# Kernel tuning notes

Hardware: AMD Instinct MI355X
Metric: run time of the kernel (lower is better)

The kernel has to match this reference:

```python
import jax, jax.numpy as jnp
import numpy as np

NEG_SLOPE = 0.2  # PyG GATConv leaky_relu slope


def _gat_layer(x, src, dst, W, a_src, a_dst, b, concat, num_nodes):
    # x: [N, F_in], W: [F_in, H*C], a_src/a_dst: [H, C], b: [H*C] or [C]
    H, C = a_src.shape
    h = (x @ W).reshape(num_nodes, H, C)                      # [N, H, C]
    s_src = jnp.einsum('nhc,hc->nh', h, a_src)                # [N, H]
    s_dst = jnp.einsum('nhc,hc->nh', h, a_dst)                # [N, H]
    e = jax.nn.leaky_relu(s_src[src] + s_dst[dst], NEG_SLOPE) # [E, H]
    # segment softmax over edges sharing a destination node
    m = jax.ops.segment_max(e, dst, num_segments=num_nodes)
    m = jnp.where(jnp.isfinite(m), m, 0.0)
    p = jnp.exp(e - m[dst])
    z = jax.ops.segment_sum(p, dst, num_segments=num_nodes)
    alpha = p / (z[dst] + 1e-16)                              # [E, H]
    msg = h[src] * alpha[:, :, None]                          # [E, H, C]
    out = jax.ops.segment_sum(msg, dst, num_segments=num_nodes)  # [N, H, C]
    out = out.reshape(num_nodes, H * C) if concat else out.mean(axis=1)
    return out + b


def setup_inputs() -> dict:
    key = jax.random.key(0)
    ks = jax.random.split(key, 16)
    N, E, F = 100000, 800000, 128
    H, C = 4, 32
    sc_in = 1.0 / np.sqrt(F)
    inp = {
        'x': jax.random.normal(ks[0], (N, F), jnp.float32),
        'edge_index': jax.random.randint(ks[1], (2, E), 0, N, jnp.int64),
        'W1': jax.random.normal(ks[2], (F, H * C), jnp.float32) * sc_in,
        'a_src1': jax.random.normal(ks[3], (H, C), jnp.float32),
        'a_dst1': jax.random.normal(ks[4], (H, C), jnp.float32),
        'b1': jax.random.normal(ks[5], (H * C,), jnp.float32) * 0.01,
        'W2': jax.random.normal(ks[6], (F, H * C), jnp.float32) * sc_in,
        'a_src2': jax.random.normal(ks[7], (H, C), jnp.float32),
        'a_dst2': jax.random.normal(ks[8], (H, C), jnp.float32),
        'b2': jax.random.normal(ks[9], (H * C,), jnp.float32) * 0.01,
        'W3': jax.random.normal(ks[10], (F, H * F), jnp.float32) * sc_in,
        'a_src3': jax.random.normal(ks[11], (H, F), jnp.float32),
        'a_dst3': jax.random.normal(ks[12], (H, F), jnp.float32),
        'b3': jax.random.normal(ks[13], (F,), jnp.float32) * 0.01,
    }
    return inp


def reference(x, edge_index, W1, a_src1, a_dst1, b1, W2, a_src2, a_dst2, b2,
              W3, a_src3, a_dst3, b3):
    N = x.shape[0]
    # PyG GATConv default: add self loops
    loop = jnp.arange(N, dtype=edge_index.dtype)
    src = jnp.concatenate([edge_index[0], loop])
    dst = jnp.concatenate([edge_index[1], loop])
    # conv1 (concat heads) + residual + ELU
    x1 = jax.nn.elu(_gat_layer(x, src, dst, W1, a_src1, a_dst1, b1, True, N) + x)
    # intermediate conv (concat heads) + residual + ELU
    x2 = jax.nn.elu(_gat_layer(x1, src, dst, W2, a_src2, a_dst2, b2, True, N) + x1)
    # final conv (mean over heads) + residual, no ELU
    x3 = _gat_layer(x2, src, dst, W3, a_src3, a_dst3, b3, False, N) + x2
    return x3
```

## Files before the change

kernel.cpp:

```cpp
#include <hip/hip_runtime.h>
#include <hip/hip_bf16.h>
#include <cstdint>

#define NEG_SLOPE 0.2f

typedef __bf16 bf16x8 __attribute__((ext_vector_type(8)));
typedef _Float16 half8 __attribute__((ext_vector_type(8)));
typedef float  floatx4 __attribute__((ext_vector_type(4)));

__device__ __forceinline__ float us2f(unsigned short u) {
    union { unsigned int i; float f; } c; c.i = ((unsigned int)u) << 16; return c.f;
}
__device__ __forceinline__ unsigned short f2us(float f) {
    union { float f; unsigned int i; } c; c.f = f;
    unsigned int x = c.i;
    unsigned int r = (x + 0x7fffu + ((x >> 16) & 1u)) >> 16;
    return (unsigned short)r;
}
__device__ __forceinline__ unsigned short f2h(float f) {
    union { _Float16 h; unsigned short u; } c; c.h = (_Float16)f; return c.u;
}
__device__ __forceinline__ float h2f(unsigned short u) {
    union { _Float16 h; unsigned short u; } c; c.u = u; return (float)c.h;
}
__device__ __forceinline__ float ldx(const void* p, int i, int bf) {
    return bf ? us2f(((const unsigned short*)p)[i]) : ((const float*)p)[i];
}
__device__ __forceinline__ void split2(float f, unsigned short& h, unsigned short& l) {
    h = f2us(f);
    l = f2us(f - us2f(h));
}
__device__ __forceinline__ float sel4(const float* a, int i) {
    float lo = (i & 1) ? a[1] : a[0];
    float hi = (i & 1) ? a[3] : a[2];
    return (i & 2) ? hi : lo;
}
__device__ __forceinline__ void fma4(float w, uint2 u,
                                     float& a0, float& a1, float& a2, float& a3) {
    union { unsigned int i; float f; } t0, t1, t2, t3;
    t0.i = u.x << 16; t1.i = u.x & 0xffff0000u;
    t2.i = u.y << 16; t3.i = u.y & 0xffff0000u;
    a0 = fmaf(w, t0.f, a0); a1 = fmaf(w, t1.f, a1);
    a2 = fmaf(w, t2.f, a2); a3 = fmaf(w, t3.f, a3);
}

__global__ void k_detect(const unsigned short* __restrict__ x16,
                         const unsigned int* __restrict__ ei,
                         int* __restrict__ flags) {
    if (threadIdx.x == 0 && blockIdx.x == 0) {
        int cnt = 0;
        for (int i = 0; i < 1024; ++i) {
            const unsigned short u = x16[2 * i];
            const int e = (u >> 7) & 0xFF;
            if (e < 100 || e > 160) ++cnt;
        }
        flags[0] = (cnt < 256) ? 1 : 0;
        int is64 = 1;
        for (int i = 0; i < 64; ++i)
            if (ei[2 * i + 1] != 0u) { is64 = 0; break; }
        flags[1] = is64;
    }
}

__device__ __forceinline__ int edge_at(const void* ei, int f64, long long idx) {
    if (f64) return (int)((const long long*)ei)[idx];
    return ((const int*)ei)[idx];
}

__global__ void k_hist(const void* __restrict__ ei, const int* __restrict__ flags,
                       int* __restrict__ deg, int E, int N) {
    const int f64 = flags[1];
    const int EP = E + N;
    for (int e = blockIdx.x * blockDim.x + threadIdx.x; e < EP; e += gridDim.x * blockDim.x) {
        int dst = (e < E) ? edge_at(ei, f64, (long long)E + e) : (e - E);
        atomicAdd(&deg[dst], 1);
    }
}

__global__ __launch_bounds__(1024) void k_scan_a(const int* __restrict__ deg,
                                                 int* __restrict__ coff,
                                                 int* __restrict__ part, int N) {
    __shared__ int tmp[1024];
    const int t = threadIdx.x, idx = blockIdx.x * 1024 + t;
    const int v = (idx < N) ? deg[idx] : 0;
    tmp[t] = v; __syncthreads();
    for (int s = 1; s < 1024; s <<= 1) {
        int a = (t >= s) ? tmp[t - s] : 0;
        __syncthreads(); tmp[t] += a; __syncthreads();
    }
    if (idx < N) coff[idx] = tmp[t] - v;
    if (t == 1023) part[blockIdx.x] = tmp[1023];
}

__global__ __launch_bounds__(1024) void k_scan_b(int* __restrict__ part,
                                                 int* __restrict__ coff, int nblk, int N) {
    __shared__ int tmp[1024];
    const int t = threadIdx.x;
    const int v = (t < nblk) ? part[t] : 0;
    tmp[t] = v; __syncthreads();
    for (int s = 1; s < 1024; s <<= 1) {
        int a = (t >= s) ? tmp[t - s] : 0;
        __syncthreads(); tmp[t] += a; __syncthreads();
    }
    if (t < nblk) part[t] = tmp[t] - v;
    if (t == 1023) coff[N] = tmp[1023];
}

__global__ __launch_bounds__(1024) void k_scan_c(int* __restrict__ coff,
                                                 const int* __restrict__ part, int N) {
    const int idx = blockIdx.x * 1024 + threadIdx.x;
    if (idx < N) coff[idx] += part[blockIdx.x];
}

__global__ void k_scatter(const void* __restrict__ ei, const int* __restrict__ flags,
                          const int* __restrict__ coff, int* __restrict__ cpos,
                          int* __restrict__ csrc, int E, int N) {
    const int f64 = flags[1];
    const int EP = E + N;
    for (int e = blockIdx.x * blockDim.x + threadIdx.x; e < EP; e += gridDim.x * blockDim.x) {
        int src, dst;
        if (e < E) { src = edge_at(ei, f64, e); dst = edge_at(ei, f64, (long long)E + e); }
        else       { src = dst = e - E; }
        const int p = atomicAdd(&cpos[dst], 1);
        csrc[coff[dst] + p] = src;
    }
}

template <int F16>
__global__ void k_wfrag(const void* __restrict__ Wv, const int* __restrict__ flags,
                        int wstride, int total,
                        unsigned short* __restrict__ outH, unsigned short* __restrict__ outL) {
    const int bf = flags[0];
    for (int tid = blockIdx.x * blockDim.x + threadIdx.x; tid < total;
         tid += gridDim.x * blockDim.x) {
        const int j    = tid & 7;
        const int lane = (tid >> 3) & 63;
        const int ks   = (tid >> 9) & 3;
        const int ntg  = (tid >> 11) & 7;
        const int blk  = tid >> 14;
        const int k = ks * 32 + (lane >> 4) * 8 + j;
        const int c = blk * 128 + ntg * 16 + (lane & 15);
        const float v = ldx(Wv, k * wstride + c, bf);
        unsigned short h, l;
        if (F16) {
            h = f2h(v);
            l = f2h(v - h2f(h));
        } else {
            split2(v, h, l);
        }
        outH[tid] = h; outL[tid] = l;
    }
}

__global__ void k_wa(const void* __restrict__ W, const void* __restrict__ as,
                     const void* __restrict__ ad, const int* __restrict__ flags,
                     float* __restrict__ va) {
    const int bf = flags[0];
    const int t = blockIdx.x * blockDim.x + threadIdx.x;
    if (t >= 512) return;
    const int k = t >> 2, h = t & 3;
    float ss = 0.f, dd = 0.f;
    for (int c = 0; c < 128; ++c) {
        const float w = ldx(W, k * 512 + h * 128 + c, bf);
        ss = fmaf(w, ldx(as, h * 128 + c, bf), ss);
        dd = fmaf(w, ldx(ad, h * 128 + c, bf), dd);
    }
    va[k * 8 + h] = ss;
    va[k * 8 + 4 + h] = dd;
}

template <bool XRAW, int SC>
__global__ __launch_bounds__(256) void k_gemm(const void* __restrict__ Xv,
                                              const unsigned short* __restrict__ whfB,
                                              const unsigned short* __restrict__ wlfB,
                                              unsigned short* __restrict__ Y16, int ystride,
                                              float* __restrict__ ssrc,
                                              float* __restrict__ sdst,
                                              const void* __restrict__ a_src,
                                              const void* __restrict__ a_dst,
                                              const int* __restrict__ flags,
                                              int N) {
    __shared__ __align__(16) unsigned short Ah[64][136], Al[64][136];
    __shared__ float sred[2][4][SC ? 64 : 1];
    const int bf   = flags[0];
    const int t    = threadIdx.x;
    const int row0 = blockIdx.x * 64;
    const int hy   = blockIdx.y;
    const unsigned short* whf = whfB + hy * 16384;
    const unsigned short* wlf = wlfB + hy * 16384;
    const int ycol0 = hy * 128;
    const int wv   = t >> 6;
    const int lane = t & 63;
    const int quad = lane >> 4;
    const int l16  = lane & 15;

#pragma unroll
    for (int it = 0; it < 8; ++it) {
        const int id = it * 256 + t;
        const int r  = id >> 5;
        const int c  = (id & 31) * 4;
        const int gr = row0 + r;
        ushort4 h4 = make_ushort4(0, 0, 0, 0), l4 = make_ushort4(0, 0, 0, 0);
        if (gr < N) {
            if (XRAW && bf) {
                h4 = *(const ushort4*)&((const unsigned short*)Xv)[(size_t)gr * 128 + c];
            } else {
                const float4 f = *(const float4*)&((const float*)Xv)[(size_t)gr * 128 + c];
                split2(f.x, h4.x, l4.x); split2(f.y, h4.y, l4.y);
                split2(f.z, h4.z, l4.z); split2(f.w, h4.w, l4.w);
            }
        }
        *(ushort4*)&Ah[r][c] = h4;
        *(ushort4*)&Al[r][c] = l4;
    }
    __syncthreads();

    floatx4 acc[4][2];
#pragma unroll
    for (int mt = 0; mt < 4; ++mt)
#pragma unroll
        for (int nt = 0; nt < 2; ++nt) acc[mt][nt] = (floatx4){0.f, 0.f, 0.f, 0.f};

#pragma unroll
    for (int ks = 0; ks < 4; ++ks) {
        const int ko = ks * 32 + quad * 8;
        bf16x8 ah[4], al[4], bh[2], bl[2];
#pragma unroll
        for (int mt = 0; mt < 4; ++mt) ah[mt] = *(const bf16x8*)&Ah[mt * 16 + l16][ko];
        if (!(XRAW && bf)) {
#pragma unroll
            for (int mt = 0; mt < 4; ++mt) al[mt] = *(const bf16x8*)&Al[mt * 16 + l16][ko];
        }
#pragma unroll
        for (int nt = 0; nt < 2; ++nt)
            bh[nt] = *(const bf16x8*)&whf[(((wv * 2 + nt) * 4 + ks) * 64 + lane) * 8];
        if (!bf) {
#pragma unroll
            for (int nt = 0; nt < 2; ++nt)
                bl[nt] = *(const bf16x8*)&wlf[(((wv * 2 + nt) * 4 + ks) * 64 + lane) * 8];
        }
#pragma unroll
        for (int mt = 0; mt < 4; ++mt)
#pragma unroll
            for (int nt = 0; nt < 2; ++nt) {
                acc[mt][nt] = __builtin_amdgcn_mfma_f32_16x16x32_bf16(ah[mt], bh[nt], acc[mt][nt], 0, 0, 0);
                if (!bf)
                    acc[mt][nt] = __builtin_amdgcn_mfma_f32_16x16x32_bf16(ah[mt], bl[nt], acc[mt][nt], 0, 0, 0);
                if (!(XRAW && bf))
                    acc[mt][nt] = __builtin_amdgcn_mfma_f32_16x16x32_bf16(al[mt], bh[nt], acc[mt][nt], 0, 0, 0);
            }
    }

    const int aBase = hy * 128 + wv * 32;
    float as_[2], ad_[2];
#pragma unroll
    for (int nt = 0; nt < 2; ++nt) {
        as_[nt] = ldx(a_src, aBase + nt * 16 + l16, bf);
        ad_[nt] = ldx(a_dst, aBase + nt * 16 + l16, bf);
    }

#pragma unroll
    for (int mt = 0; mt < 4; ++mt) {
        const int rl = mt * 16 + quad * 4;
#pragma unroll
        for (int r = 0; r < 4; ++r) {
            const int grow = row0 + rl + r;
            if (grow < N) {
#pragma unroll
                for (int nt = 0; nt < 2; ++nt)
                    Y16[(size_t)grow * ystride + ycol0 + wv * 32 + nt * 16 + l16] =
                        f2us(acc[mt][nt][r]);
            }
            float ps = acc[mt][0][r] * as_[0] + acc[mt][1][r] * as_[1];
            float pd = acc[mt][0][r] * ad_[0] + acc[mt][1][r] * ad_[1];
#pragma unroll
            for (int mk = 1; mk <= 8; mk <<= 1) {
                ps += __shfl_xor(ps, mk);
                pd += __shfl_xor(pd, mk);
            }
            if (SC == 0) {
                if (l16 == 0 && grow < N) {
                    ssrc[(size_t)grow * 4 + wv] = ps;
                    sdst[(size_t)grow * 4 + wv] = pd;
                }
            } else {
                if (l16 == 0) { sred[0][wv][rl + r] = ps; sred[1][wv][rl + r] = pd; }
            }
        }
    }
    if (SC == 1) {
        __syncthreads();
        if (t < 64 && row0 + t < N) {
            ssrc[(size_t)(row0 + t) * 4 + hy] = sred[0][0][t] + sred[0][1][t] + sred[0][2][t] + sred[0][3][t];
            sdst[(size_t)(row0 + t) * 4 + hy] = sred[1][0][t] + sred[1][1][t] + sred[1][2][t] + sred[1][3][t];
        }
    }
}

template <int MODE>
__global__ __launch_bounds__(256) void k_agg(const int* __restrict__ coff,
                                             const int* __restrict__ csrc,
                                             const float* __restrict__ ssrc,
                                             const float* __restrict__ sdst,
                                             const unsigned short* __restrict__ H16,
                                             const void* __restrict__ bias,
                                             const void* __restrict__ resid,
                                             const int* __restrict__ flags,
                                             void* __restrict__ out, int N,
                                             const float* __restrict__ va,
                                             float* __restrict__ ss2,
                                             float* __restrict__ sd2,
                                             unsigned short* __restrict__ x2h) {
    __shared__ int   sS[4][64];
    __shared__ float wS[4][256];
    __shared__ float vaS[(MODE == 1) ? 128 : 1][9];
    const int bf   = flags[0];
    const int wv   = threadIdx.x >> 6;
    const int lane = threadIdx.x & 63;
    const int n0   = blockIdx.x * 4 + wv;
    const bool nact = n0 < N;
    const int n    = nact ? n0 : (N - 1);
    const int beg = coff[n], end = coff[n + 1];
    const int deg = end - beg;

    if (MODE == 1) {
        for (int i = threadIdx.x; i < 1024; i += 256) vaS[i >> 3][i & 7] = va[i];
    }

    const float4 sdv = *(const float4*)&sdst[(size_t)n * 4];
    float sd[4] = { sdv.x, sdv.y, sdv.z, sdv.w };

    const bool fast = (deg <= 64);
    float m[4], z[4];

    if (fast) {
        const bool act = lane < deg;
        int myS = 0;
        float v[4];
#pragma unroll
        for (int h = 0; h < 4; ++h) v[h] = -1e30f;
        if (act) {
            myS = csrc[beg + lane];
            const float4 sp = *(const float4*)&ssrc[(size_t)myS * 4];
            const float s4[4] = { sp.x, sp.y, sp.z, sp.w };
#pragma unroll
            for (int h = 0; h < 4; ++h) {
                float tv = s4[h] + sd[h];
                v[h] = tv >= 0.f ? tv : NEG_SLOPE * tv;
            }
        }
#pragma unroll
        for (int h = 0; h < 4; ++h) m[h] = v[h];
#pragma unroll
        for (int mk = 1; mk <= 32; mk <<= 1)
#pragma unroll
            for (int h = 0; h < 4; ++h) m[h] = fmaxf(m[h], __shfl_xor(m[h], mk));
        float w[4];
#pragma unroll
        for (int h = 0; h < 4; ++h) w[h] = act ? expf(v[h] - m[h]) : 0.f;
#pragma unroll
        for (int h = 0; h < 4; ++h) z[h] = w[h];
#pragma unroll
        for (int mk = 1; mk <= 32; mk <<= 1)
#pragma unroll
            for (int h = 0; h < 4; ++h) z[h] += __shfl_xor(z[h], mk);
        if (act) {
            sS[wv][lane] = myS;
#pragma unroll
            for (int h = 0; h < 4; ++h)
                wS[wv][lane * 4 + h] = w[h] / (z[h] + 1e-16f);
        }
    } else {
#pragma unroll
        for (int h = 0; h < 4; ++h) m[h] = -1e30f;
        for (int e = beg + lane; e < end; e += 64) {
            const int s = csrc[e];
            const float4 sp = *(const float4*)&ssrc[(size_t)s * 4];
            const float s4[4] = { sp.x, sp.y, sp.z, sp.w };
#pragma unroll
            for (int h = 0; h < 4; ++h) {
                float tv = s4[h] + sd[h];
                tv = tv >= 0.f ? tv : NEG_SLOPE * tv;
                m[h] = fmaxf(m[h], tv);
            }
        }
#pragma unroll
        for (int mk = 1; mk <= 32; mk <<= 1)
#pragma unroll
            for (int h = 0; h < 4; ++h) m[h] = fmaxf(m[h], __shfl_xor(m[h], mk));
#pragma unroll
        for (int h = 0; h < 4; ++h) z[h] = 0.f;
        for (int e = beg + lane; e < end; e += 64) {
            const int s = csrc[e];
            const float4 sp = *(const float4*)&ssrc[(size_t)s * 4];
            const float s4[4] = { sp.x, sp.y, sp.z, sp.w };
#pragma unroll
            for (int h = 0; h < 4; ++h) {
                float tv = s4[h] + sd[h];
                tv = tv >= 0.f ? tv : NEG_SLOPE * tv;
                z[h] += expf(tv - m[h]);
            }
        }
#pragma unroll
        for (int mk = 1; mk <= 32; mk <<= 1)
#pragma unroll
            for (int h = 0; h < 4; ++h) z[h] += __shfl_xor(z[h], mk);
    }

    __syncthreads();

    const int half = lane >> 5;
    const int l32  = lane & 31;
    const int c4   = l32 * 4;
    const int hd   = l32 >> 3;
    float a0 = 0.f, a1 = 0.f, a2 = 0.f, a3 = 0.f;

    if (fast) {
        for (int e0 = 0; e0 < deg; e0 += 2) {
            const int e = e0 + half;
            if (e < deg) {
                const int s = sS[wv][e];
                const float w = wS[wv][e * 4 + hd];
                const uint2 u = *(const uint2*)&H16[(size_t)s * 128 + c4];
                fma4(w, u, a0, a1, a2, a3);
            }
        }
    } else {
        float ivh[4];
#pragma unroll
        for (int h = 0; h < 4; ++h) ivh[h] = 1.f / (z[h] + 1e-16f);
        const float mh = sel4(m, hd), sdh = sel4(sd, hd), ih = sel4(ivh, hd);
        for (int e0 = 0; e0 < deg; e0 += 2) {
            const int e = e0 + half;
            if (e < deg) {
                const int s = csrc[beg + e];
                float tv = ssrc[(size_t)s * 4 + hd] + sdh;
                tv = tv >= 0.f ? tv : NEG_SLOPE * tv;
                const float w = expf(tv - mh) * ih;
                const uint2 u = *(const uint2*)&H16[(size_t)s * 128 + c4];
                fma4(w, u, a0, a1, a2, a3);
            }
        }
    }

    a0 += __shfl_xor(a0, 32);
    a1 += __shfl_xor(a1, 32);
    a2 += __shfl_xor(a2, 32);
    a3 += __shfl_xor(a3, 32);

    if (half != 0 || !nact) return;
    const int ob = n * 128 + c4;
    const float vv[4] = { a0, a1, a2, a3 };
    float rr[4];
    if (MODE == 0) {
#pragma unroll
        for (int i = 0; i < 4; ++i) rr[i] = ldx(resid, ob + i, bf);
    } else {
        const float4 r4 = *(const float4*)&((const float*)resid)[ob];
        rr[0] = r4.x; rr[1] = r4.y; rr[2] = r4.z; rr[3] = r4.w;
    }
    float o[4];
#pragma unroll
    for (int i = 0; i < 4; ++i) {
        const float v = vv[i] + ldx(bias, c4 + i, bf) + rr[i];
        o[i] = v > 0.f ? v : expm1f(v);
    }
    float4 o4 = make_float4(o[0], o[1], o[2], o[3]);
    *(float4*)&((float*)out)[ob] = o4;

    if (MODE == 1) {
        ushort4 u16;
        u16.x = f2us(o[0]); u16.y = f2us(o[1]); u16.z = f2us(o[2]); u16.w = f2us(o[3]);
        *(ushort4*)&x2h[ob] = u16;
        float p[8];
#pragma unroll
        for (int o8 = 0; o8 < 8; ++o8)
            p[o8] = fmaf(o[0], vaS[c4 + 0][o8],
                    fmaf(o[1], vaS[c4 + 1][o8],
                    fmaf(o[2], vaS[c4 + 2][o8], o[3] * vaS[c4 + 3][o8])));
#pragma unroll
        for (int mk = 1; mk <= 16; mk <<= 1)
#pragma unroll
            for (int o8 = 0; o8 < 8; ++o8) p[o8] += __shfl_xor(p[o8], mk);
        if (l32 == 0) {
#pragma unroll
            for (int h = 0; h < 4; ++h) {
                ss2[(size_t)n * 4 + h] = p[h];
                sd2[(size_t)n * 4 + h] = p[4 + h];
            }
        }
    }
}

__global__ __launch_bounds__(256) void k_aggx(const int* __restrict__ coff,
                                              const int* __restrict__ csrc,
                                              const float* __restrict__ ssrc,
                                              const float* __restrict__ sdst,
                                              const unsigned short* __restrict__ X16,
                                              unsigned short* __restrict__ aggO,
                                              int N) {
    __shared__ int   sS[4][64];
    __shared__ float wS[4][256];
    const int wv   = threadIdx.x >> 6;
    const int lane = threadIdx.x & 63;
    const int n0   = blockIdx.x * 4 + wv;
    const bool nact = n0 < N;
    const int n    = nact ? n0 : (N - 1);
    const int beg = coff[n], end = coff[n + 1];
    const int deg = end - beg;

    const float4 sdv = *(const float4*)&sdst[(size_t)n * 4];
    float sd[4] = { sdv.x, sdv.y, sdv.z, sdv.w };

    const bool fast = (deg <= 64);
    float m[4], z[4];

    if (fast) {
        const bool act = lane < deg;
        int myS = 0;
        float v[4];
#pragma unroll
        for (int h = 0; h < 4; ++h) v[h] = -1e30f;
        if (act) {
            myS = csrc[beg + lane];
            const float4 sp = *(const float4*)&ssrc[(size_t)myS * 4];
            const float s4[4] = { sp.x, sp.y, sp.z, sp.w };
#pragma unroll
            for (int h = 0; h < 4; ++h) {
                float tv = s4[h] + sd[h];
                v[h] = tv >= 0.f ? tv : NEG_SLOPE * tv;
            }
        }
#pragma unroll
        for (int h = 0; h < 4; ++h) m[h] = v[h];
#pragma unroll
        for (int mk = 1; mk <= 32; mk <<= 1)
#pragma unroll
            for (int h = 0; h < 4; ++h) m[h] = fmaxf(m[h], __shfl_xor(m[h], mk));
        float w[4];
#pragma unroll
        for (int h = 0; h < 4; ++h) w[h] = act ? expf(v[h] - m[h]) : 0.f;
#pragma unroll
        for (int h = 0; h < 4; ++h) z[h] = w[h];
#pragma unroll
        for (int mk = 1; mk <= 32; mk <<= 1)
#pragma unroll
            for (int h = 0; h < 4; ++h) z[h] += __shfl_xor(z[h], mk);
        if (act) {
            sS[wv][lane] = myS;
#pragma unroll
            for (int h = 0; h < 4; ++h)
                wS[wv][lane * 4 + h] = w[h] / (z[h] + 1e-16f);
        }
    } else {
#pragma unroll
        for (int h = 0; h < 4; ++h) m[h] = -1e30f;
        for (int e = beg + lane; e < end; e += 64) {
            const int s = csrc[e];
            const float4 sp = *(const float4*)&ssrc[(size_t)s * 4];
            const float s4[4] = { sp.x, sp.y, sp.z, sp.w };
#pragma unroll
            for (int h = 0; h < 4; ++h) {
                float tv = s4[h] + sd[h];
                tv = tv >= 0.f ? tv : NEG_SLOPE * tv;
                m[h] = fmaxf(m[h], tv);
            }
        }
#pragma unroll
        for (int mk = 1; mk <= 32; mk <<= 1)
#pragma unroll
            for (int h = 0; h < 4; ++h) m[h] = fmaxf(m[h], __shfl_xor(m[h], mk));
#pragma unroll
        for (int h = 0; h < 4; ++h) z[h] = 0.f;
        for (int e = beg + lane; e < end; e += 64) {
            const int s = csrc[e];
            const float4 sp = *(const float4*)&ssrc[(size_t)s * 4];
            const float s4[4] = { sp.x, sp.y, sp.z, sp.w };
#pragma unroll
            for (int h = 0; h < 4; ++h) {
                float tv = s4[h] + sd[h];
                tv = tv >= 0.f ? tv : NEG_SLOPE * tv;
                z[h] += expf(tv - m[h]);
            }
        }
#pragma unroll
        for (int mk = 1; mk <= 32; mk <<= 1)
#pragma unroll
            for (int h = 0; h < 4; ++h) z[h] += __shfl_xor(z[h], mk);
    }

    __syncthreads();

    const int half = lane >> 5;
    const int l32  = lane & 31;
    const int c4   = l32 * 4;
    float ac[4][4];
#pragma unroll
    for (int h = 0; h < 4; ++h)
#pragma unroll
        for (int j = 0; j < 4; ++j) ac[h][j] = 0.f;

    if (fast) {
        for (int e0 = 0; e0 < deg; e0 += 2) {
            const int e = e0 + half;
            if (e < deg) {
                const int s = sS[wv][e];
                const float4 w4 = *(const float4*)&wS[wv][e * 4];
                const float wr[4] = { w4.x, w4.y, w4.z, w4.w };
                const uint2 u = *(const uint2*)&X16[(size_t)s * 128 + c4];
                union { unsigned int i; float f; } t0, t1, t2, t3;
                t0.i = u.x << 16; t1.i = u.x & 0xffff0000u;
                t2.i = u.y << 16; t3.i = u.y & 0xffff0000u;
#pragma unroll
                for (int h = 0; h < 4; ++h) {
                    ac[h][0] = fmaf(wr[h], t0.f, ac[h][0]);
                    ac[h][1] = fmaf(wr[h], t1.f, ac[h][1]);
                    ac[h][2] = fmaf(wr[h], t2.f, ac[h][2]);
                    ac[h][3] = fmaf(wr[h], t3.f, ac[h][3]);
                }
            }
        }
    } else {
        float ivh[4];
#pragma unroll
        for (int h = 0; h < 4; ++h) ivh[h] = 1.f / (z[h] + 1e-16f);
        for (int e0 = 0; e0 < deg; e0 += 2) {
            const int e = e0 + half;
            if (e < deg) {
                const int s = csrc[beg + e];
                const float4 sp = *(const float4*)&ssrc[(size_t)s * 4];
                const float s4[4] = { sp.x, sp.y, sp.z, sp.w };
                float wr[4];
#pragma unroll
                for (int h = 0; h < 4; ++h) {
                    float tv = s4[h] + sd[h];
                    tv = tv >= 0.f ? tv : NEG_SLOPE * tv;
                    wr[h] = expf(tv - m[h]) * ivh[h];
                }
                const uint2 u = *(const uint2*)&X16[(size_t)s * 128 + c4];
                union { unsigned int i; float f; } t0, t1, t2, t3;
                t0.i = u.x << 16; t1.i = u.x & 0xffff0000u;
                t2.i = u.y << 16; t3.i = u.y & 0xffff0000u;
#pragma unroll
                for (int h = 0; h < 4; ++h) {
                    ac[h][0] = fmaf(wr[h], t0.f, ac[h][0]);
                    ac[h][1] = fmaf(wr[h], t1.f, ac[h][1]);
                    ac[h][2] = fmaf(wr[h], t2.f, ac[h][2]);
                    ac[h][3] = fmaf(wr[h], t3.f, ac[h][3]);
                }
            }
        }
    }

#pragma unroll
    for (int h = 0; h < 4; ++h)
#pragma unroll
        for (int j = 0; j < 4; ++j) ac[h][j] += __shfl_xor(ac[h][j], 32);

    if (half != 0 || !nact) return;
#pragma unroll
    for (int h = 0; h < 4; ++h) {
        ushort4 o;
        o.x = f2h(ac[h][0]); o.y = f2h(ac[h][1]);
        o.z = f2h(ac[h][2]); o.w = f2h(ac[h][3]);
        *(ushort4*)&aggO[(size_t)n0 * 512 + h * 128 + c4] = o;
    }
}

__global__ __launch_bounds__(256) void k_gemm3(const unsigned short* __restrict__ A16,
                                               const unsigned short* __restrict__ whf,
                                               const unsigned short* __restrict__ wlf,
                                               const void* __restrict__ bias,
                                               const float* __restrict__ resid,
                                               const int* __restrict__ flags,
                                               void* __restrict__ out, int N) {
    __shared__ __align__(16) unsigned short Ah[64][136];
    const int bf   = flags[0];
    const int t    = threadIdx.x;
    const int row0 = blockIdx.x * 64;
    const int wv   = t >> 6;
    const int lane = t & 63;
    const int quad = lane >> 4;
    const int l16  = lane & 15;

    floatx4 acc[4][2];
#pragma unroll
    for (int mt = 0; mt < 4; ++mt)
#pragma unroll
        for (int nt = 0; nt < 2; ++nt) acc[mt][nt] = (floatx4){0.f, 0.f, 0.f, 0.f};

    for (int kc = 0; kc < 4; ++kc) {
        if (kc) __syncthreads();
#pragma unroll
        for (int it = 0; it < 8; ++it) {
            const int id = it * 256 + t;
            const int r  = id >> 5;
            const int c  = (id & 31) * 4;
            ushort4 h4 = make_ushort4(0, 0, 0, 0);
            if (row0 + r < N)
                h4 = *(const ushort4*)&A16[(size_t)(row0 + r) * 512 + kc * 128 + c];
            *(ushort4*)&Ah[r][c] = h4;
        }
        __syncthreads();

        const unsigned short* whc = whf + kc * 16384;
        const unsigned short* wlc = wlf + kc * 16384;
#pragma unroll
        for (int ks = 0; ks < 4; ++ks) {
            const int ko = ks * 32 + quad * 8;
            half8 ah[4], bh[2], bl[2];
#pragma unroll
            for (int mt = 0; mt < 4; ++mt) ah[mt] = *(const half8*)&Ah[mt * 16 + l16][ko];
#pragma unroll
            for (int nt = 0; nt < 2; ++nt) {
                bh[nt] = *(const half8*)&whc[(((wv * 2 + nt) * 4 + ks) * 64 + lane) * 8];
                bl[nt] = *(const half8*)&wlc[(((wv * 2 + nt) * 4 + ks) * 64 + lane) * 8];
            }
#pragma unroll
            for (int mt = 0; mt < 4; ++mt)
#pragma unroll
                for (int nt = 0; nt < 2; ++nt) {
                    acc[mt][nt] = __builtin_amdgcn_mfma_f32_16x16x32_f16(ah[mt], bh[nt], acc[mt][nt], 0, 0, 0);
                    acc[mt][nt] = __builtin_amdgcn_mfma_f32_16x16x32_f16(ah[mt], bl[nt], acc[mt][nt], 0, 0, 0);
                }
        }
    }

#pragma unroll
    for (int mt = 0; mt < 4; ++mt) {
        const int rl = mt * 16 + quad * 4;
#pragma unroll
        for (int r = 0; r < 4; ++r) {
            const int grow = row0 + rl + r;
            if (grow < N) {
#pragma unroll
                for (int nt = 0; nt < 2; ++nt) {
                    const int col = wv * 32 + nt * 16 + l16;
                    const float v = acc[mt][nt][r] * 0.25f + ldx(bias, col, bf)
                                  + resid[(size_t)grow * 128 + col];
                    if (bf) ((unsigned short*)out)[(size_t)grow * 128 + col] = f2us(v);
                    else    ((float*)out)[(size_t)grow * 128 + col] = v;
                }
            }
        }
    }
}

extern "C" void kernel_launch(void* const* d_in, const int* in_sizes, int n_in,
                              void* d_out, int out_size, void* d_ws, size_t ws_size,
                              hipStream_t stream) {
    const int N  = in_sizes[0] / 128;
    const int E  = in_sizes[1] / 2;
    const int EP = E + N;

    const void* x   = d_in[0];
    const void* ei  = d_in[1];
    const void* W1  = d_in[2];
    const void* as1 = d_in[3];
    const void* ad1 = d_in[4];
    const void* b1  = d_in[5];
    const void* W2  = d_in[6];
    const void* as2 = d_in[7];
    const void* ad2 = d_in[8];
    const void* b2  = d_in[9];
    const void* W3  = d_in[10];
    const void* as3 = d_in[11];
    const void* ad3 = d_in[12];
    const void* b3  = d_in[13];

    char* p = (char*)d_ws;
    auto alloc = [&](size_t bytes) { char* r = p; p += (bytes + 255) & ~(size_t)255; return r; };
    int*   flags = (int*)alloc(8);
    int*   deg   = (int*)alloc((size_t)(N + 1) * 4);
    int*   coff  = (int*)alloc((size_t)(N + 1) * 4);
    int*   cpos  = (int*)alloc((size_t)N * 4);
    int*   part  = (int*)alloc(4096);
    int*   csrc  = (int*)alloc((size_t)EP * 4);
    char*  region = alloc((size_t)N * 512 * 2);
    float* x2b   = (float*)alloc((size_t)N * 128 * 4);
    float* ssrc  = (float*)alloc((size_t)N * 4 * 4);
    float* sdst  = (float*)alloc((size_t)N * 4 * 4);
    unsigned short* whf1 = (unsigned short*)alloc(16384 * 2);
    unsigned short* wlf1 = (unsigned short*)alloc(16384 * 2);
    unsigned short* whf2 = (unsigned short*)alloc(16384 * 2);
    unsigned short* wlf2 = (unsigned short*)alloc(16384 * 2);
    unsigned short* whf3 = (unsigned short*)alloc(65536 * 2);
    unsigned short* wlf3 = (unsigned short*)alloc(65536 * 2);
    unsigned short* x2h  = (unsigned short*)alloc((size_t)N * 128 * 2);
    float* va    = (float*)alloc(128 * 8 * 4);
    float* ssrc3 = (float*)alloc((size_t)N * 4 * 4);
    float* sdst3 = (float*)alloc((size_t)N * 4 * 4);

    float*          x1b    = (float*)region;
    unsigned short* h16_12 = (unsigned short*)(region + (size_t)N * 128 * 4);
    unsigned short* aggF   = (unsigned short*)region;

    hipMemsetAsync(deg,  0, (size_t)(N + 1) * 4, stream);
    hipMemsetAsync(cpos, 0, (size_t)N * 4, stream);

    k_detect<<<1, 64, 0, stream>>>((const unsigned short*)x, (const unsigned int*)ei, flags);

    k_wfrag<0><<<64, 256, 0, stream>>>(W1, flags, 128, 16384, whf1, wlf1);
    k_wfrag<0><<<64, 256, 0, stream>>>(W2, flags, 128, 16384, whf2, wlf2);
    k_wfrag<1><<<256, 256, 0, stream>>>(W3, flags, 512, 65536, whf3, wlf3);
    k_wa<<<2, 256, 0, stream>>>(W3, as3, ad3, flags, va);

    const int egrid = (EP + 255) / 256;
    const int nblk  = (N + 1023) / 1024;
    k_hist<<<egrid, 256, 0, stream>>>(ei, flags, deg, E, N);
    k_scan_a<<<nblk, 1024, 0, stream>>>(deg, coff, part, N);
    k_scan_b<<<1, 1024, 0, stream>>>(part, coff, nblk, N);
    k_scan_c<<<nblk, 1024, 0, stream>>>(coff, part, N);
    k_scatter<<<egrid, 256, 0, stream>>>(ei, flags, coff, cpos, csrc, E, N);

    const int ggrid = (N + 63) / 64;
    const int ngrid = (N + 3) / 4;

    k_gemm<true, 0><<<dim3(ggrid, 1), 256, 0, stream>>>(x, whf1, wlf1, h16_12, 128,
                                                        ssrc, sdst, as1, ad1, flags, N);
    k_agg<0><<<ngrid, 256, 0, stream>>>(coff, csrc, ssrc, sdst, h16_12, b1, x, flags, x1b, N,
                                        nullptr, nullptr, nullptr, nullptr);

    k_gemm<false, 0><<<dim3(ggrid, 1), 256, 0, stream>>>(x1b, whf2, wlf2, h16_12, 128,
                                                         ssrc, sdst, as2, ad2, flags, N);
    k_agg<1><<<ngrid, 256, 0, stream>>>(coff, csrc, ssrc, sdst, h16_12, b2, x1b, flags, x2b, N,
                                        va, ssrc3, sdst3, x2h);

    k_aggx<<<ngrid, 256, 0, stream>>>(coff, csrc, ssrc3, sdst3, x2h, aggF, N);
    k_gemm3<<<ggrid, 256, 0, stream>>>(aggF, whf3, wlf3, b3, x2b, flags, d_out, N);
}
```

Before: 751.7 us.

## Map each destination node to 16 lanes with 8-wide loads in aggregation kernels

The aggregation kernels (k_agg, k_aggx) now handle each destination node with 16 lanes, so a block covers 16 nodes instead of 4. Each lane loads 8 bf16 features per neighbor with a 16-byte load, and edge indices and weights are broadcast through width-16 shuffles instead of shared memory. This removes the shared-memory staging, the block barrier and the cross-half reduction. With an average degree near 9, fewer lanes sit idle and more rows are in flight per wave. In exchange, each lane runs a serial loop over all neighbors, the fast path only covers degree up to 16, and k_aggx needs 32 accumulators per lane, which raises register pressure.

Measured after the change: 686.8 us. 8.6% less time.

```diff
diff --git a/kernel.cpp b/kernel.cpp
--- a/kernel.cpp
+++ b/kernel.cpp
@@ -35,13 +35,16 @@
     float hi = (i & 1) ? a[3] : a[2];
     return (i & 2) ? hi : lo;
 }
-__device__ __forceinline__ void fma4(float w, uint2 u,
-                                     float& a0, float& a1, float& a2, float& a3) {
-    union { unsigned int i; float f; } t0, t1, t2, t3;
-    t0.i = u.x << 16; t1.i = u.x & 0xffff0000u;
-    t2.i = u.y << 16; t3.i = u.y & 0xffff0000u;
-    a0 = fmaf(w, t0.f, a0); a1 = fmaf(w, t1.f, a1);
-    a2 = fmaf(w, t2.f, a2); a3 = fmaf(w, t3.f, a3);
+__device__ __forceinline__ void unp8(uint4 u, float* f) {
+    union { unsigned int i; float ff; } a;
+    a.i = u.x << 16;          f[0] = a.ff;
+    a.i = u.x & 0xffff0000u;  f[1] = a.ff;
+    a.i = u.y << 16;          f[2] = a.ff;
+    a.i = u.y & 0xffff0000u;  f[3] = a.ff;
+    a.i = u.z << 16;          f[4] = a.ff;
+    a.i = u.z & 0xffff0000u;  f[5] = a.ff;
+    a.i = u.w << 16;          f[6] = a.ff;
+    a.i = u.w & 0xffff0000u;  f[7] = a.ff;
 }
 
 __global__ void k_detect(const unsigned short* __restrict__ x16,
@@ -311,36 +314,35 @@
                                              float* __restrict__ ss2,
                                              float* __restrict__ sd2,
                                              unsigned short* __restrict__ x2h) {
-    __shared__ int   sS[4][64];
-    __shared__ float wS[4][256];
     __shared__ float vaS[(MODE == 1) ? 128 : 1][9];
     const int bf   = flags[0];
-    const int wv   = threadIdx.x >> 6;
-    const int lane = threadIdx.x & 63;
-    const int n0   = blockIdx.x * 4 + wv;
+    const int t    = threadIdx.x;
+    const int l16  = t & 15;
+    const int n0   = blockIdx.x * 16 + (t >> 4);
     const bool nact = n0 < N;
     const int n    = nact ? n0 : (N - 1);
     const int beg = coff[n], end = coff[n + 1];
     const int deg = end - beg;
 
     if (MODE == 1) {
-        for (int i = threadIdx.x; i < 1024; i += 256) vaS[i >> 3][i & 7] = va[i];
+        for (int i = t; i < 1024; i += 256) vaS[i >> 3][i & 7] = va[i];
+        __syncthreads();
     }
 
     const float4 sdv = *(const float4*)&sdst[(size_t)n * 4];
-    float sd[4] = { sdv.x, sdv.y, sdv.z, sdv.w };
-
-    const bool fast = (deg <= 64);
+    const float sd[4] = { sdv.x, sdv.y, sdv.z, sdv.w };
+    const bool fast = (deg <= 16);
     float m[4], z[4];
+    int   myS = 0;
+    float wn[4] = { 0.f, 0.f, 0.f, 0.f };
 
     if (fast) {
-        const bool act = lane < deg;
-        int myS = 0;
+        const bool act = l16 < deg;
         float v[4];
 #pragma unroll
         for (int h = 0; h < 4; ++h) v[h] = -1e30f;
         if (act) {
-            myS = csrc[beg + lane];
+            myS = csrc[beg + l16];
             const float4 sp = *(const float4*)&ssrc[(size_t)myS * 4];
             const float s4[4] = { sp.x, sp.y, sp.z, sp.w };
 #pragma unroll
@@ -352,7 +354,7 @@
 #pragma unroll
         for (int h = 0; h < 4; ++h) m[h] = v[h];
 #pragma unroll
-        for (int mk = 1; mk <= 32; mk <<= 1)
+        for (int mk = 1; mk <= 8; mk <<= 1)
 #pragma unroll
             for (int h = 0; h < 4; ++h) m[h] = fmaxf(m[h], __shfl_xor(m[h], mk));
         float w[4];
@@ -361,19 +363,15 @@
 #pragma unroll
         for (int h = 0; h < 4; ++h) z[h] = w[h];
 #pragma unroll
-        for (int mk = 1; mk <= 32; mk <<= 1)
+        for (int mk = 1; mk <= 8; mk <<= 1)
 #pragma unroll
             for (int h = 0; h < 4; ++h) z[h] += __shfl_xor(z[h], mk);
-        if (act) {
-            sS[wv][lane] = myS;
-#pragma unroll
-            for (int h = 0; h < 4; ++h)
-                wS[wv][lane * 4 + h] = w[h] / (z[h] + 1e-16f);
-        }
+#pragma unroll
+        for (int h = 0; h < 4; ++h) wn[h] = w[h] / (z[h] + 1e-16f);
     } else {
 #pragma unroll
         for (int h = 0; h < 4; ++h) m[h] = -1e30f;
-        for (int e = beg + lane; e < end; e += 64) {
+        for (int e = beg + l16; e < end; e += 16) {
             const int s = csrc[e];
             const float4 sp = *(const float4*)&ssrc[(size_t)s * 4];
             const float s4[4] = { sp.x, sp.y, sp.z, sp.w };
@@ -385,12 +383,12 @@
             }
         }
 #pragma unroll
-        for (int mk = 1; mk <= 32; mk <<= 1)
+        for (int mk = 1; mk <= 8; mk <<= 1)
 #pragma unroll
             for (int h = 0; h < 4; ++h) m[h] = fmaxf(m[h], __shfl_xor(m[h], mk));
 #pragma unroll
         for (int h = 0; h < 4; ++h) z[h] = 0.f;
-        for (int e = beg + lane; e < end; e += 64) {
+        for (int e = beg + l16; e < end; e += 16) {
             const int s = csrc[e];
             const float4 sp = *(const float4*)&ssrc[(size_t)s * 4];
             const float s4[4] = { sp.x, sp.y, sp.z, sp.w };
@@ -402,87 +400,96 @@
             }
         }
 #pragma unroll
-        for (int mk = 1; mk <= 32; mk <<= 1)
+        for (int mk = 1; mk <= 8; mk <<= 1)
 #pragma unroll
             for (int h = 0; h < 4; ++h) z[h] += __shfl_xor(z[h], mk);
     }
 
-    __syncthreads();
-
-    const int half = lane >> 5;
-    const int l32  = lane & 31;
-    const int c4   = l32 * 4;
-    const int hd   = l32 >> 3;
-    float a0 = 0.f, a1 = 0.f, a2 = 0.f, a3 = 0.f;
+    const int c8 = l16 * 8;
+    const int hd = l16 >> 2;
+    float ac[8];
+#pragma unroll
+    for (int j = 0; j < 8; ++j) ac[j] = 0.f;
 
     if (fast) {
-        for (int e0 = 0; e0 < deg; e0 += 2) {
-            const int e = e0 + half;
-            if (e < deg) {
-                const int s = sS[wv][e];
-                const float w = wS[wv][e * 4 + hd];
-                const uint2 u = *(const uint2*)&H16[(size_t)s * 128 + c4];
-                fma4(w, u, a0, a1, a2, a3);
-            }
+        for (int e = 0; e < deg; ++e) {
+            const int s = __shfl(myS, e, 16);
+            float wa4[4];
+            wa4[0] = __shfl(wn[0], e, 16);
+            wa4[1] = __shfl(wn[1], e, 16);
+            wa4[2] = __shfl(wn[2], e, 16);
+            wa4[3] = __shfl(wn[3], e, 16);
+            const float w = sel4(wa4, hd);
+            const uint4 u = *(const uint4*)&H16[(size_t)s * 128 + c8];
+            float f[8]; unp8(u, f);
+#pragma unroll
+            for (int j = 0; j < 8; ++j) ac[j] = fmaf(w, f[j], ac[j]);
         }
     } else {
         float ivh[4];
 #pragma unroll
         for (int h = 0; h < 4; ++h) ivh[h] = 1.f / (z[h] + 1e-16f);
         const float mh = sel4(m, hd), sdh = sel4(sd, hd), ih = sel4(ivh, hd);
-        for (int e0 = 0; e0 < deg; e0 += 2) {
-            const int e = e0 + half;
-            if (e < deg) {
-                const int s = csrc[beg + e];
-                float tv = ssrc[(size_t)s * 4 + hd] + sdh;
-                tv = tv >= 0.f ? tv : NEG_SLOPE * tv;
-                const float w = expf(tv - mh) * ih;
-                const uint2 u = *(const uint2*)&H16[(size_t)s * 128 + c4];
-                fma4(w, u, a0, a1, a2, a3);
-            }
-        }
-    }
-
-    a0 += __shfl_xor(a0, 32);
-    a1 += __shfl_xor(a1, 32);
-    a2 += __shfl_xor(a2, 32);
-    a3 += __shfl_xor(a3, 32);
-
-    if (half != 0 || !nact) return;
-    const int ob = n * 128 + c4;
-    const float vv[4] = { a0, a1, a2, a3 };
-    float rr[4];
+        for (int e = beg; e < end; ++e) {
+            const int s = csrc[e];
+            float tv = ssrc[(size_t)s * 4 + hd] + sdh;
+            tv = tv >= 0.f ? tv : NEG_SLOPE * tv;
+            const float w = expf(tv - mh) * ih;
+            const uint4 u = *(const uint4*)&H16[(size_t)s * 128 + c8];
+            float f[8]; unp8(u, f);
+#pragma unroll
+            for (int j = 0; j < 8; ++j) ac[j] = fmaf(w, f[j], ac[j]);
+        }
+    }
+
+    if (!nact) return;
+    const int ob = n * 128 + c8;
+    float rr[8];
     if (MODE == 0) {
-#pragma unroll
-        for (int i = 0; i < 4; ++i) rr[i] = ldx(resid, ob + i, bf);
+        if (bf) {
+            const uint4 u = *(const uint4*)&((const unsigned short*)resid)[ob];
+            unp8(u, rr);
+        } else {
+            const float4 r0 = *(const float4*)&((const float*)resid)[ob];
+            const float4 r1 = *(const float4*)&((const float*)resid)[ob + 4];
+            rr[0] = r0.x; rr[1] = r0.y; rr[2] = r0.z; rr[3] = r0.w;
+            rr[4] = r1.x; rr[5] = r1.y; rr[6] = r1.z; rr[7] = r1.w;
+        }
     } else {
-        const float4 r4 = *(const float4*)&((const float*)resid)[ob];
-        rr[0] = r4.x; rr[1] = r4.y; rr[2] = r4.z; rr[3] = r4.w;
-    }
-    float o[4];
-#pragma unroll
-    for (int i = 0; i < 4; ++i) {
-        const float v = vv[i] + ldx(bias, c4 + i, bf) + rr[i];
-        o[i] = v > 0.f ? v : expm1f(v);
-    }
-    float4 o4 = make_float4(o[0], o[1], o[2], o[3]);
-    *(float4*)&((float*)out)[ob] = o4;
+        const float4 r0 = *(const float4*)&((const float*)resid)[ob];
+        const float4 r1 = *(const float4*)&((const float*)resid)[ob + 4];
+        rr[0] = r0.x; rr[1] = r0.y; rr[2] = r0.z; rr[3] = r0.w;
+        rr[4] = r1.x; rr[5] = r1.y; rr[6] = r1.z; rr[7] = r1.w;
+    }
+    float o[8];
+#pragma unroll
+    for (int j = 0; j < 8; ++j) {
+        const float v = ac[j] + ldx(bias, c8 + j, bf) + rr[j];
+        o[j] = v > 0.f ? v : expm1f(v);
+    }
+    *(float4*)&((float*)out)[ob]     = make_float4(o[0], o[1], o[2], o[3]);
+    *(float4*)&((float*)out)[ob + 4] = make_float4(o[4], o[5], o[6], o[7]);
 
     if (MODE == 1) {
-        ushort4 u16;
-        u16.x = f2us(o[0]); u16.y = f2us(o[1]); u16.z = f2us(o[2]); u16.w = f2us(o[3]);
-        *(ushort4*)&x2h[ob] = u16;
+        uint4 u16;
+        u16.x = (unsigned int)f2us(o[0]) | ((unsigned int)f2us(o[1]) << 16);
+        u16.y = (unsigned int)f2us(o[2]) | ((unsigned int)f2us(o[3]) << 16);
+        u16.z = (unsigned int)f2us(o[4]) | ((unsigned int)f2us(o[5]) << 16);
+        u16.w = (unsigned int)f2us(o[6]) | ((unsigned int)f2us(o[7]) << 16);
+        *(uint4*)&x2h[ob] = u16;
         float p[8];
 #pragma unroll
-        for (int o8 = 0; o8 < 8; ++o8)
-            p[o8] = fmaf(o[0], vaS[c4 + 0][o8],
-                    fmaf(o[1], vaS[c4 + 1][o8],
-                    fmaf(o[2], vaS[c4 + 2][o8], o[3] * vaS[c4 + 3][o8])));
-#pragma unroll
-        for (int mk = 1; mk <= 16; mk <<= 1)
+        for (int o8 = 0; o8 < 8; ++o8) {
+            float acc = 0.f;
+#pragma unroll
+            for (int j = 0; j < 8; ++j) acc = fmaf(o[j], vaS[c8 + j][o8], acc);
+            p[o8] = acc;
+        }
+#pragma unroll
+        for (int mk = 1; mk <= 8; mk <<= 1)
 #pragma unroll
             for (int o8 = 0; o8 < 8; ++o8) p[o8] += __shfl_xor(p[o8], mk);
-        if (l32 == 0) {
+        if (l16 == 0) {
 #pragma unroll
             for (int h = 0; h < 4; ++h) {
                 ss2[(size_t)n * 4 + h] = p[h];
@@ -499,30 +506,28 @@
                                               const unsigned short* __restrict__ X16,
                                               unsigned short* __restrict__ aggO,
                                               int N) {
-    __shared__ int   sS[4][64];
-    __shared__ float wS[4][256];
-    const int wv   = threadIdx.x >> 6;
-    const int lane = threadIdx.x & 63;
-    const int n0   = blockIdx.x * 4 + wv;
+    const int t    = threadIdx.x;
+    const int l16  = t & 15;
+    const int n0   = blockIdx.x * 16 + (t >> 4);
     const bool nact = n0 < N;
     const int n    = nact ? n0 : (N - 1);
     const int beg = coff[n], end = coff[n + 1];
     const int deg = end - beg;
 
     const float4 sdv = *(const float4*)&sdst[(size_t)n * 4];
-    float sd[4] = { sdv.x, sdv.y, sdv.z, sdv.w };
-
-    const bool fast = (deg <= 64);
+    const float sd[4] = { sdv.x, sdv.y, sdv.z, sdv.w };
+    const bool fast = (deg <= 16);
     float m[4], z[4];
+    int   myS = 0;
+    float wn[4] = { 0.f, 0.f, 0.f, 0.f };
 
     if (fast) {
-        const bool act = lane < deg;
-        int myS = 0;
+        const bool act = l16 < deg;
         float v[4];
 #pragma unroll
         for (int h = 0; h < 4; ++h) v[h] = -1e30f;
         if (act) {
-            myS = csrc[beg + lane];
+            myS = csrc[beg + l16];
             const float4 sp = *(const float4*)&ssrc[(size_t)myS * 4];
             const float s4[4] = { sp.x, sp.y, sp.z, sp.w };
 #pragma unroll
@@ -534,7 +539,7 @@
 #pragma unroll
         for (int h = 0; h < 4; ++h) m[h] = v[h];
 #pragma unroll
-        for (int mk = 1; mk <= 32; mk <<= 1)
+        for (int mk = 1; mk <= 8; mk <<= 1)
 #pragma unroll
             for (int h = 0; h < 4; ++h) m[h] = fmaxf(m[h], __shfl_xor(m[h], mk));
         float w[4];
@@ -543,19 +548,15 @@
 #pragma unroll
         for (int h = 0; h < 4; ++h) z[h] = w[h];
 #pragma unroll
-        for (int mk = 1; mk <= 32; mk <<= 1)
+        for (int mk = 1; mk <= 8; mk <<= 1)
 #pragma unroll
             for (int h = 0; h < 4; ++h) z[h] += __shfl_xor(z[h], mk);
-        if (act) {
-            sS[wv][lane] = myS;
-#pragma unroll
-            for (int h = 0; h < 4; ++h)
-                wS[wv][lane * 4 + h] = w[h] / (z[h] + 1e-16f);
-        }
+#pragma unroll
+        for (int h = 0; h < 4; ++h) wn[h] = w[h] / (z[h] + 1e-16f);
     } else {
 #pragma unroll
         for (int h = 0; h < 4; ++h) m[h] = -1e30f;
-        for (int e = beg + lane; e < end; e += 64) {
+        for (int e = beg + l16; e < end; e += 16) {
             const int s = csrc[e];
             const float4 sp = *(const float4*)&ssrc[(size_t)s * 4];
             const float s4[4] = { sp.x, sp.y, sp.z, sp.w };
@@ -567,12 +568,12 @@
             }
         }
 #pragma unroll
-        for (int mk = 1; mk <= 32; mk <<= 1)
+        for (int mk = 1; mk <= 8; mk <<= 1)
 #pragma unroll
             for (int h = 0; h < 4; ++h) m[h] = fmaxf(m[h], __shfl_xor(m[h], mk));
 #pragma unroll
         for (int h = 0; h < 4; ++h) z[h] = 0.f;
-        for (int e = beg + lane; e < end; e += 64) {
+        for (int e = beg + l16; e < end; e += 16) {
             const int s = csrc[e];
             const float4 sp = *(const float4*)&ssrc[(size_t)s * 4];
             const float s4[4] = { sp.x, sp.y, sp.z, sp.w };
@@ -584,86 +585,66 @@
             }
         }
 #pragma unroll
-        for (int mk = 1; mk <= 32; mk <<= 1)
+        for (int mk = 1; mk <= 8; mk <<= 1)
 #pragma unroll
             for (int h = 0; h < 4; ++h) z[h] += __shfl_xor(z[h], mk);
     }
 
-    __syncthreads();
-
-    const int half = lane >> 5;
-    const int l32  = lane & 31;
-    const int c4   = l32 * 4;
-    float ac[4][4];
+    const int c8 = l16 * 8;
+    float ac[4][8];
 #pragma unroll
     for (int h = 0; h < 4; ++h)
 #pragma unroll
-        for (int j = 0; j < 4; ++j) ac[h][j] = 0.f;
+        for (int j = 0; j < 8; ++j) ac[h][j] = 0.f;
 
     if (fast) {
-        for (int e0 = 0; e0 < deg; e0 += 2) {
-            const int e = e0 + half;
-            if (e < deg) {
-                const int s = sS[wv][e];
-                const float4 w4 = *(const float4*)&wS[wv][e * 4];
-                const float wr[4] = { w4.x, w4.y, w4.z, w4.w };
-                const uint2 u = *(const uint2*)&X16[(size_t)s * 128 + c4];
-                union { unsigned int i; float f; } t0, t1, t2, t3;
-                t0.i = u.x << 16; t1.i = u.x & 0xffff0000u;
-                t2.i = u.y << 16; t3.i = u.y & 0xffff0000u;
-#pragma unroll
-                for (int h = 0; h < 4; ++h) {
-                    ac[h][0] = fmaf(wr[h], t0.f, ac[h][0]);
-                    ac[h][1] = fmaf(wr[h], t1.f, ac[h][1]);
-                    ac[h][2] = fmaf(wr[h], t2.f, ac[h][2]);
-                    ac[h][3] = fmaf(wr[h], t3.f, ac[h][3]);
-                }
-            }
+        for (int e = 0; e < deg; ++e) {
+            const int s = __shfl(myS, e, 16);
+            float wr[4];
+            wr[0] = __shfl(wn[0], e, 16);
+            wr[1] = __shfl(wn[1], e, 16);
+            wr[2] = __shfl(wn[2], e, 16);
+            wr[3] = __shfl(wn[3], e, 16);
+            const uint4 u = *(const uint4*)&X16[(size_t)s * 128 + c8];
+            float f[8]; unp8(u, f);
+#pragma unroll
+            for (int h = 0; h < 4; ++h)
+#pragma unroll
+                for (int j = 0; j < 8; ++j) ac[h][j] = fmaf(wr[h], f[j], ac[h][j]);
         }
     } else {
         float ivh[4];
 #pragma unroll
         for (int h = 0; h < 4; ++h) ivh[h] = 1.f / (z[h] + 1e-16f);
-        for (int e0 = 0; e0 < deg; e0 += 2) {
-            const int e = e0 + half;
-            if (e < deg) {
-                const int s = csrc[beg + e];
-                const float4 sp = *(const float4*)&ssrc[(size_t)s * 4];
-                const float s4[4] = { sp.x, sp.y, sp.z, sp.w };
-                float wr[4];
-#pragma unroll
-                for (int h = 0; h < 4; ++h) {
-                    float tv = s4[h] + sd[h];
-                    tv = tv >= 0.f ? tv : NEG_SLOPE * tv;
-                    wr[h] = expf(tv - m[h]) * ivh[h];
-                }
-                const uint2 u = *(const uint2*)&X16[(size_t)s * 128 + c4];
-                union { unsigned int i; float f; } t0, t1, t2, t3;
-                t0.i = u.x << 16; t1.i = u.x & 0xffff0000u;
-                t2.i = u.y << 16; t3.i = u.y & 0xffff0000u;
-#pragma unroll
-                for (int h = 0; h < 4; ++h) {
-                    ac[h][0] = fmaf(wr[h], t0.f, ac[h][0]);
-                    ac[h][1] = fmaf(wr[h], t1.f, ac[h][1]);
-                    ac[h][2] = fmaf(wr[h], t2.f, ac[h][2]);
-                    ac[h][3] = fmaf(wr[h], t3.f, ac[h][3]);
-                }
-            }
-        }
-    }
-
-#pragma unroll
-    for (int h = 0; h < 4; ++h)
-#pragma unroll
-        for (int j = 0; j < 4; ++j) ac[h][j] += __shfl_xor(ac[h][j], 32);
-
-    if (half != 0 || !nact) return;
+        for (int e = beg; e < end; ++e) {
+            const int s = csrc[e];
+            const float4 sp = *(const float4*)&ssrc[(size_t)s * 4];
+            const float s4[4] = { sp.x, sp.y, sp.z, sp.w };
+            float wr[4];
+#pragma unroll
+            for (int h = 0; h < 4; ++h) {
+                float tv = s4[h] + sd[h];
+                tv = tv >= 0.f ? tv : NEG_SLOPE * tv;
+                wr[h] = expf(tv - m[h]) * ivh[h];
+            }
+            const uint4 u = *(const uint4*)&X16[(size_t)s * 128 + c8];
+            float f[8]; unp8(u, f);
+#pragma unroll
+            for (int h = 0; h < 4; ++h)
+#pragma unroll
+                for (int j = 0; j < 8; ++j) ac[h][j] = fmaf(wr[h], f[j], ac[h][j]);
+        }
+    }
+
+    if (!nact) return;
 #pragma unroll
     for (int h = 0; h < 4; ++h) {
-        ushort4 o;
-        o.x = f2h(ac[h][0]); o.y = f2h(ac[h][1]);
-        o.z = f2h(ac[h][2]); o.w = f2h(ac[h][3]);
-        *(ushort4*)&aggO[(size_t)n0 * 512 + h * 128 + c4] = o;
+        uint4 u;
+        u.x = (unsigned int)f2h(ac[h][0]) | ((unsigned int)f2h(ac[h][1]) << 16);
+        u.y = (unsigned int)f2h(ac[h][2]) | ((unsigned int)f2h(ac[h][3]) << 16);
+        u.z = (unsigned int)f2h(ac[h][4]) | ((unsigned int)f2h(ac[h][5]) << 16);
+        u.w = (unsigned int)f2h(ac[h][6]) | ((unsigned int)f2h(ac[h][7]) << 16);
+        *(uint4*)&aggO[(size_t)n0 * 512 + h * 128 + c8] = u;
     }
 }
 
@@ -814,7 +795,7 @@
     k_scatter<<<egrid, 256, 0, stream>>>(ei, flags, coff, cpos, csrc, E, N);
 
     const int ggrid = (N + 63) / 64;
-    const int ngrid = (N + 3) / 4;
+    const int ngrid = (N + 15) / 16;
 
     k_gemm<true, 0><<<dim3(ggrid, 1), 256, 0, stream>>>(x, whf1, wlf1, h16_12, 128,
                                                         ssrc, sdst, as1, ad1, flags, N);
```
